# Optimization experiments

Measured on AMD Instinct MI355X. Metric: run time of the kernel, lower is better.

## Reference

```python
import jax, jax.numpy as jnp
import numpy as np

N = 100000      # num_nodes
FEAT = 256      # num_features
H = 128         # hidden
C = 40          # num_classes
K = 4           # hops
RWS = 10        # random-walk samples per node
NL = 2          # nlayer
ALPHA = 0.1


def setup_inputs() -> dict:
    key = jax.random.key(0)
    ks = jax.random.split(key, 10)
    x = jax.random.normal(ks[0], (N, FEAT), dtype=jnp.float32)
    degree = jax.random.uniform(ks[1], (N,), minval=1.0, maxval=64.0, dtype=jnp.float32)
    # precomputed random-walk endpoints per layer per hop: [NL, K, N*RWS]
    ends = jax.random.randint(ks[2], (NL, K, N * RWS), 0, N, dtype=jnp.int32)
    # att init: alpha*(1-alpha)^k, last entry (1-alpha)^K, tiled per layer
    a = ALPHA * (1.0 - ALPHA) ** jnp.arange(K + 1, dtype=jnp.float32)
    a = a.at[-1].set((1.0 - ALPHA) ** K)
    att = jnp.tile(a[None, :], (NL, 1))
    def lin(k, fan_in, fan_out):
        s = 1.0 / np.sqrt(fan_in)
        return jax.random.uniform(k, (fan_in, fan_out), minval=-s, maxval=s, dtype=jnp.float32)
    W0 = lin(ks[3], FEAT, H)
    b0 = jnp.zeros((H,), dtype=jnp.float32)
    W1 = lin(ks[4], H, H)
    b1 = jnp.zeros((H,), dtype=jnp.float32)
    W2 = lin(ks[5], H, C)
    b2 = jnp.zeros((C,), dtype=jnp.float32)
    return {"x": x, "degree": degree, "ends": ends, "att": att,
            "W0": W0, "b0": b0, "W1": W1, "b1": b1, "W2": W2, "b2": b2}


def reference(x, degree, ends, att, W0, b0, W1, b1, W2, b2):
    Ws = [(W0, b0), (W1, b1)]
    starts = jnp.repeat(jnp.arange(N), RWS)          # [N*RWS] walk start node ids
    d_sqrt = jnp.sqrt(degree)                        # degree^0.5
    d_isqrt = jax.lax.rsqrt(degree)                  # degree^-0.5
    h = x
    for i in range(NL):
        W, b = Ws[i]
        h = h @ W + b                                # Linear (dropout p=0)
        mask = att[i]                                # [K+1]
        agg = h * mask[0]
        for k in range(1, K + 1):
            e = ends[i, k - 1]                       # [N*RWS] hop-k endpoints
            w = d_sqrt[starts] * d_isqrt[e]          # degree reweighting
            samp = (w[:, None] * h[e]).reshape(N, RWS, h.shape[1]).mean(axis=1)
            agg = agg + samp * mask[k]
        h = jax.nn.relu(agg)
    logits = h @ W2 + b2
    return jax.nn.log_softmax(logits, axis=1)
```

## Files before the change

kernel.cpp:

```cpp
#include <hip/hip_runtime.h>
#include <math.h>

#define NNODES 100000
#define NFEAT  256
#define HID    128
#define NCLS   40
#define KHOP   4
#define RWSAMP 10
#define KP1    5

typedef __bf16 bf16;
typedef __attribute__((ext_vector_type(8)))  __bf16 bf16x8;
typedef __attribute__((ext_vector_type(2)))  float  f32x2;
typedef __attribute__((ext_vector_type(16))) float  f32x16;

typedef __attribute__((address_space(3))) unsigned       lds_u32;
typedef __attribute__((address_space(1))) const unsigned glb_u32;

__global__ __launch_bounds__(256) void prep_w(
    const float* __restrict__ W0, const float* __restrict__ W1,
    const float* __restrict__ W2,
    bf16* __restrict__ Wt0, bf16* __restrict__ Wt1, bf16* __restrict__ Wt2)
{
    int tid = blockIdx.x * 256 + threadIdx.x;
    if (tid < 128 * 256) {
        int n = tid >> 8, k = tid & 255;
        Wt0[tid] = (bf16)W0[k * 128 + n];
    } else if (tid < 128 * 256 + 128 * 128) {
        int i = tid - 128 * 256;
        int n = i >> 7, k = i & 127;
        Wt1[i] = (bf16)W1[k * 128 + n];
    } else if (tid < 128 * 256 + 128 * 128 + 64 * 128) {
        int i = tid - (128 * 256 + 128 * 128);
        int n = i >> 7, k = i & 127;
        Wt2[i] = (n < NCLS) ? (bf16)W2[k * NCLS + n] : (bf16)0.0f;
    }
}

template<int K, bool A_BF16>
__global__ __launch_bounds__(256) void gemm_nodes(
    const void* __restrict__ Av, const bf16* __restrict__ Wt,
    const float* __restrict__ bias, unsigned char* __restrict__ F8, int M)
{
    constexpr int BK  = 128;
    constexpr int LDB = BK + 4;
    __shared__ bf16 Bs[128 * LDB];
    __shared__ bf16 As[4][32 * LDB];

    const int tid  = threadIdx.x;
    const int wv   = tid >> 6;
    const int lane = tid & 63;
    const int l31  = lane & 31;
    const int lhi  = lane >> 5;
    const int blockRow = blockIdx.x * 128;
    const int rowBase  = blockRow + wv * 32;

    const bf16*  Ab = (const bf16*)Av;
    const float* Af = (const float*)Av;

    f32x16 acc[4];
#pragma unroll
    for (int t = 0; t < 4; ++t)
#pragma unroll
        for (int r = 0; r < 16; ++r) acc[t][r] = 0.0f;

    for (int k0 = 0; k0 < K; k0 += BK) {
        if (k0) __syncthreads();
#pragma unroll 4
        for (int l = 0; l < 8; ++l) {
            int c   = tid + l * 256;
            int row = c >> 4;
            int kc  = (c & 15) * 8;
            uint4 v = *(const uint4*)(Wt + (size_t)row * K + k0 + kc);
            *(uint2*)&Bs[row * LDB + kc]     = make_uint2(v.x, v.y);
            *(uint2*)&Bs[row * LDB + kc + 4] = make_uint2(v.z, v.w);
        }
        __syncthreads();

        if (A_BF16) {
#pragma unroll 4
            for (int l = 0; l < 8; ++l) {
                int c  = lane + l * 64;
                int r  = c >> 4;
                int kc = (c & 15) * 8;
                int gr = min(rowBase + r, M - 1);
                uint4 v = *(const uint4*)(Ab + (size_t)gr * K + k0 + kc);
                *(uint2*)&As[wv][r * LDB + kc]     = make_uint2(v.x, v.y);
                *(uint2*)&As[wv][r * LDB + kc + 4] = make_uint2(v.z, v.w);
            }
        } else {
#pragma unroll 4
            for (int l = 0; l < 16; ++l) {
                int c  = lane + l * 64;
                int r  = c >> 5;
                int kc = (c & 31) * 4;
                int gr = min(rowBase + r, M - 1);
                float4 v = *(const float4*)(Af + (size_t)gr * K + k0 + kc);
                union { bf16 h[4]; uint2 u; } t4;
                t4.h[0] = (bf16)v.x; t4.h[1] = (bf16)v.y;
                t4.h[2] = (bf16)v.z; t4.h[3] = (bf16)v.w;
                *(uint2*)&As[wv][r * LDB + kc] = t4.u;
            }
        }

#pragma unroll
        for (int ks = 0; ks < BK / 16; ++ks) {
            const int ko = ks * 16 + lhi * 8;
            union { uint2 u2[2]; bf16x8 v; } ua, ub;
            ua.u2[0] = *(const uint2*)&As[wv][l31 * LDB + ko];
            ua.u2[1] = *(const uint2*)&As[wv][l31 * LDB + ko + 4];
            bf16x8 a = ua.v;
#pragma unroll
            for (int t = 0; t < 4; ++t) {
                ub.u2[0] = *(const uint2*)&Bs[(t * 32 + l31) * LDB + ko];
                ub.u2[1] = *(const uint2*)&Bs[(t * 32 + l31) * LDB + ko + 4];
                acc[t] = __builtin_amdgcn_mfma_f32_32x32x16_bf16(a, ub.v, acc[t], 0, 0, 0);
            }
        }
    }

    __syncthreads();
    unsigned* ldsq = (unsigned*)Bs;

#pragma unroll
    for (int t = 0; t < 4; ++t) {
        int col = t * 32 + l31;
        float bc = bias[col];
#pragma unroll
        for (int G = 0; G < 4; ++G) {
            float v0 = acc[t][4 * G + 0] + bc;
            float v1 = acc[t][4 * G + 1] + bc;
            float v2 = acc[t][4 * G + 2] + bc;
            float v3 = acc[t][4 * G + 3] + bc;
            int p = __builtin_amdgcn_cvt_pk_fp8_f32(v0, v1, 0, false);
            p = __builtin_amdgcn_cvt_pk_fp8_f32(v2, v3, p, true);
            ldsq[(wv * 8 + 2 * G + lhi) * 128 + col] = (unsigned)p;
        }
    }
    __syncthreads();

    {
        const int j  = tid & 31;
        const int Q0 = (tid >> 5) * 4;
#pragma unroll
        for (int qq = 0; qq < 4; ++qq) {
            int Q = Q0 + qq;
            uint4 d = *(const uint4*)&ldsq[Q * 128 + 4 * j];
            int growb = blockRow + 4 * Q;
#pragma unroll
            for (int i = 0; i < 4; ++i) {
                unsigned sel = ((unsigned)(4 + i) << 8) | (unsigned)i;
                unsigned lo = __builtin_amdgcn_perm(d.y, d.x, sel);
                unsigned hi = __builtin_amdgcn_perm(d.w, d.z, sel);
                unsigned o  = __builtin_amdgcn_perm(hi, lo, 0x05040100u);
                if (growb + i < M)
                    *(unsigned*)(F8 + (size_t)(growb + i) * 128 + 4 * j) = o;
            }
        }
    }
}

__global__ __launch_bounds__(256) void agg_relu_fp8(
    const unsigned char* __restrict__ hf8, bf16* __restrict__ hout,
    const int* __restrict__ ends, const float* __restrict__ degree,
    const float* __restrict__ att)
{
    __shared__ __attribute__((aligned(16))) unsigned char stage[4][82 * 128];
    __shared__ int   sewE[4][82];
    __shared__ float sewW[4][82];

    const int wv   = threadIdx.x >> 6;
    const int lane = threadIdx.x & 63;
    const int n0   = blockIdx.x * 8 + wv * 2;

    for (int en = lane; en < 82; en += 64) {
        int node = en > 40;
        int j = en - node * 41;
        int n = n0 + node;
        int e;
        float w;
        if (j == 40) {
            e = n;
            w = att[0];
        } else {
            int k = j / RWSAMP, s = j - k * RWSAMP;
            e = ends[(size_t)k * (NNODES * RWSAMP) + (size_t)n * RWSAMP + s];
            w = att[k + 1] * (1.0f / RWSAMP) * sqrtf(degree[n]) * rsqrtf(degree[e]);
        }
        sewE[wv][en] = e << 7;
        sewW[wv][en] = w;
    }

    {
        const unsigned char* gbase = hf8 + (unsigned)((lane & 31) * 4);
#pragma unroll
        for (int t = 0; t < 41; ++t) {
            int r = 2 * t + (lane >> 5);
            int eoff = sewE[wv][r];
            __builtin_amdgcn_global_load_lds(
                (glb_u32*)(gbase + (unsigned)eoff),
                (lds_u32*)&stage[wv][t * 256],
                4, 0, 0);
        }
    }
    asm volatile("s_waitcnt vmcnt(0)" ::: "memory");
    __builtin_amdgcn_sched_barrier(0);

    const int q  = lane >> 4;
    const int c8 = (lane & 15) * 8;

    f32x2 a0[4], a1[4];
#pragma unroll
    for (int i = 0; i < 4; ++i) { a0[i] = (f32x2){0.f, 0.f}; a1[i] = (f32x2){0.f, 0.f}; }

#pragma unroll
    for (int t = 0; t < 10; ++t) {
        int j = 4 * t + q;
        uint2 g0 = *(const uint2*)&stage[wv][j * 128 + c8];
        uint2 g1 = *(const uint2*)&stage[wv][(41 + j) * 128 + c8];
        float w0 = sewW[wv][j];
        float w1 = sewW[wv][41 + j];
        f32x2 w20 = {w0, w0}, w21 = {w1, w1};
        a0[0] = __builtin_elementwise_fma(w20, __builtin_amdgcn_cvt_pk_f32_fp8((int)g0.x, false), a0[0]);
        a0[1] = __builtin_elementwise_fma(w20, __builtin_amdgcn_cvt_pk_f32_fp8((int)g0.x, true),  a0[1]);
        a0[2] = __builtin_elementwise_fma(w20, __builtin_amdgcn_cvt_pk_f32_fp8((int)g0.y, false), a0[2]);
        a0[3] = __builtin_elementwise_fma(w20, __builtin_amdgcn_cvt_pk_f32_fp8((int)g0.y, true),  a0[3]);
        a1[0] = __builtin_elementwise_fma(w21, __builtin_amdgcn_cvt_pk_f32_fp8((int)g1.x, false), a1[0]);
        a1[1] = __builtin_elementwise_fma(w21, __builtin_amdgcn_cvt_pk_f32_fp8((int)g1.x, true),  a1[1]);
        a1[2] = __builtin_elementwise_fma(w21, __builtin_amdgcn_cvt_pk_f32_fp8((int)g1.y, false), a1[2]);
        a1[3] = __builtin_elementwise_fma(w21, __builtin_amdgcn_cvt_pk_f32_fp8((int)g1.y, true),  a1[3]);
    }

#pragma unroll
    for (int i = 0; i < 4; ++i) {
        a0[i].x += __shfl_xor(a0[i].x, 16, 64); a0[i].y += __shfl_xor(a0[i].y, 16, 64);
        a1[i].x += __shfl_xor(a1[i].x, 16, 64); a1[i].y += __shfl_xor(a1[i].y, 16, 64);
        a0[i].x += __shfl_xor(a0[i].x, 32, 64); a0[i].y += __shfl_xor(a0[i].y, 32, 64);
        a1[i].x += __shfl_xor(a1[i].x, 32, 64); a1[i].y += __shfl_xor(a1[i].y, 32, 64);
    }

    if (q < 2) {
        const int n = n0 + q;
        f32x2* a = (q == 0) ? a0 : a1;
        const int selfRow = q ? 81 : 40;
        uint2 sv = *(const uint2*)&stage[wv][selfRow * 128 + c8];
        float att0 = sewW[wv][selfRow];
        f32x2 av = {att0, att0};
        a[0] = __builtin_elementwise_fma(av, __builtin_amdgcn_cvt_pk_f32_fp8((int)sv.x, false), a[0]);
        a[1] = __builtin_elementwise_fma(av, __builtin_amdgcn_cvt_pk_f32_fp8((int)sv.x, true),  a[1]);
        a[2] = __builtin_elementwise_fma(av, __builtin_amdgcn_cvt_pk_f32_fp8((int)sv.y, false), a[2]);
        a[3] = __builtin_elementwise_fma(av, __builtin_amdgcn_cvt_pk_f32_fp8((int)sv.y, true),  a[3]);

        f32x2 z = {0.f, 0.f};
#pragma unroll
        for (int i = 0; i < 4; ++i) a[i] = __builtin_elementwise_max(a[i], z);

        union { bf16 h[8]; uint4 u; } st;
        st.h[0] = (bf16)a[0].x; st.h[1] = (bf16)a[0].y;
        st.h[2] = (bf16)a[1].x; st.h[3] = (bf16)a[1].y;
        st.h[4] = (bf16)a[2].x; st.h[5] = (bf16)a[2].y;
        st.h[6] = (bf16)a[3].x; st.h[7] = (bf16)a[3].y;
        *(uint4*)(hout + (size_t)n * HID + c8) = st.u;
    }
}

__global__ __launch_bounds__(256) void head_mfma(
    const bf16* __restrict__ h, const bf16* __restrict__ Wt2,
    const float* __restrict__ b2, float* __restrict__ out, int M)
{
    constexpr int K = HID, LDB = K + 8;
    __shared__ bf16 Bs[64 * LDB];

    const int tid = threadIdx.x;
    constexpr int CPR = K / 8;
    for (int f = tid; f < 64 * CPR; f += 256) {
        int row = f / CPR;
        int kc  = (f % CPR) * 8;
        *(uint4*)&Bs[row * LDB + kc] = *(const uint4*)(Wt2 + (size_t)row * K + kc);
    }
    __syncthreads();

    const int wv   = tid >> 6;
    const int lane = tid & 63;
    const int l31  = lane & 31;
    const int lhi  = lane >> 5;
    const int blockRow = blockIdx.x * 128;
    const int arow = min(blockRow + wv * 32 + l31, M - 1);

    f32x16 acc[2];
#pragma unroll
    for (int t = 0; t < 2; ++t)
#pragma unroll
        for (int r = 0; r < 16; ++r) acc[t][r] = 0.0f;

#pragma unroll
    for (int ks = 0; ks < K / 16; ++ks) {
        bf16x8 a = *(const bf16x8*)(h + (size_t)arow * K + ks * 16 + lhi * 8);
#pragma unroll
        for (int t = 0; t < 2; ++t) {
            bf16x8 b = *(const bf16x8*)&Bs[(t * 32 + l31) * LDB + ks * 16 + lhi * 8];
            acc[t] = __builtin_amdgcn_mfma_f32_32x32x16_bf16(a, b, acc[t], 0, 0, 0);
        }
    }

    const float bc0 = b2[l31];
    const float bc1 = (l31 < 8) ? b2[32 + l31] : 0.0f;

#pragma unroll
    for (int r = 0; r < 16; ++r) {
        float v0 = acc[0][r] + bc0;
        float v1 = (l31 < 8) ? (acc[1][r] + bc1) : -INFINITY;

        float m = fmaxf(v0, v1);
#pragma unroll
        for (int off = 16; off > 0; off >>= 1)
            m = fmaxf(m, __shfl_xor(m, off, 64));

        float s = __expf(v0 - m) + ((l31 < 8) ? __expf(v1 - m) : 0.0f);
#pragma unroll
        for (int off = 16; off > 0; off >>= 1)
            s += __shfl_xor(s, off, 64);

        float ls = __logf(s);
        int grow = blockRow + wv * 32 + (r & 3) + 8 * (r >> 2) + 4 * lhi;
        if (grow < M) {
            out[(size_t)grow * NCLS + l31] = v0 - m - ls;
            if (l31 < 8)
                out[(size_t)grow * NCLS + 32 + l31] = v1 - m - ls;
        }
    }
}

extern "C" void kernel_launch(void* const* d_in, const int* in_sizes, int n_in,
                              void* d_out, int out_size, void* d_ws, size_t ws_size,
                              hipStream_t stream)
{
    const float* x      = (const float*)d_in[0];
    const float* degree = (const float*)d_in[1];
    const int*   ends   = (const int*)  d_in[2];
    const float* att    = (const float*)d_in[3];
    const float* W0     = (const float*)d_in[4];
    const float* b0     = (const float*)d_in[5];
    const float* W1     = (const float*)d_in[6];
    const float* b1     = (const float*)d_in[7];
    const float* W2     = (const float*)d_in[8];
    const float* b2     = (const float*)d_in[9];
    float* out = (float*)d_out;

    bf16* hb0 = (bf16*)d_ws;
    bf16* hb1 = hb0 + (size_t)NNODES * HID;
    unsigned char* hf8 = (unsigned char*)(hb1 + (size_t)NNODES * HID);
    bf16* Wt0 = (bf16*)(hf8 + (size_t)NNODES * HID);
    bf16* Wt1 = Wt0 + 128 * 256;
    bf16* Wt2 = Wt1 + 128 * 128;

    const int prepN = 128 * 256 + 128 * 128 + 64 * 128;
    prep_w<<<(prepN + 255) / 256, 256, 0, stream>>>(W0, W1, W2, Wt0, Wt1, Wt2);

    const int gGemm = (NNODES + 127) / 128;
    const int gAgg  = (NNODES + 7) / 8;

    gemm_nodes<NFEAT, false><<<gGemm, 256, 0, stream>>>(x, Wt0, b0, hf8, NNODES);
    agg_relu_fp8<<<gAgg, 256, 0, stream>>>(hf8, hb1, ends, degree, att);
    gemm_nodes<HID, true><<<gGemm, 256, 0, stream>>>(hb1, Wt1, b1, hf8, NNODES);
    agg_relu_fp8<<<gAgg, 256, 0, stream>>>(
        hf8, hb0, ends + (size_t)KHOP * NNODES * RWSAMP, degree, att + KP1);
    head_mfma<<<gGemm, 256, 0, stream>>>(hb0, Wt2, b2, out, NNODES);
}
```

Baseline: 393.9 us.

## Slice fp8 features into column slabs and gather per-slice in aggregation

The GEMM epilogue now writes the fp8 hidden features as four column slices of 32 bytes per node instead of full 128-byte rows. The aggregation kernel launches four times as many blocks, one per slice, so each pass gathers from a 3.2 MB slab that is more likely to stay cache-resident. Each slice gathers with direct 8-byte global loads and a shuffle reduction, replacing the LDS staging through global_load_lds. The cost is recomputing the endpoint indices and weights four times and issuing smaller, less coalesced gather requests.

```diff
diff --git a/kernel.cpp b/kernel.cpp
--- a/kernel.cpp
+++ b/kernel.cpp
@@ -9,13 +9,14 @@
 #define RWSAMP 10
 #define KP1    5
 
+#define NSLICE 4
+#define SLB    32
+#define NBAGG  ((NNODES + 7) / 8)
+
 typedef __bf16 bf16;
 typedef __attribute__((ext_vector_type(8)))  __bf16 bf16x8;
 typedef __attribute__((ext_vector_type(2)))  float  f32x2;
 typedef __attribute__((ext_vector_type(16))) float  f32x16;
-
-typedef __attribute__((address_space(3))) unsigned       lds_u32;
-typedef __attribute__((address_space(1))) const unsigned glb_u32;
 
 __global__ __launch_bounds__(256) void prep_w(
     const float* __restrict__ W0, const float* __restrict__ W1,
@@ -142,6 +143,8 @@
     {
         const int j  = tid & 31;
         const int Q0 = (tid >> 5) * 4;
+        const int slice = j >> 3;
+        const int b4    = (j & 7) * 4;
 #pragma unroll
         for (int qq = 0; qq < 4; ++qq) {
             int Q = Q0 + qq;
@@ -154,31 +157,32 @@
                 unsigned hi = __builtin_amdgcn_perm(d.w, d.z, sel);
                 unsigned o  = __builtin_amdgcn_perm(hi, lo, 0x05040100u);
                 if (growb + i < M)
-                    *(unsigned*)(F8 + (size_t)(growb + i) * 128 + 4 * j) = o;
+                    *(unsigned*)(F8 + ((size_t)slice * NNODES + (growb + i)) * SLB + b4) = o;
             }
         }
     }
 }
 
 __global__ __launch_bounds__(256) void agg_relu_fp8(
-    const unsigned char* __restrict__ hf8, bf16* __restrict__ hout,
+    const unsigned char* __restrict__ hf8s,
+    bf16* __restrict__ hout,
     const int* __restrict__ ends, const float* __restrict__ degree,
     const float* __restrict__ att)
 {
-    __shared__ __attribute__((aligned(16))) unsigned char stage[4][82 * 128];
-    __shared__ int   sewE[4][82];
-    __shared__ float sewW[4][82];
-
-    const int wv   = threadIdx.x >> 6;
-    const int lane = threadIdx.x & 63;
-    const int n0   = blockIdx.x * 8 + wv * 2;
+    __shared__ int   sewE[4][2][41];
+    __shared__ float sewW[4][2][41];
+
+    const int slice = blockIdx.x / NBAGG;
+    const int nb    = blockIdx.x - slice * NBAGG;
+    const int wv    = threadIdx.x >> 6;
+    const int lane  = threadIdx.x & 63;
+    const int n0    = nb * 8 + wv * 2;
 
     for (int en = lane; en < 82; en += 64) {
         int node = en > 40;
         int j = en - node * 41;
         int n = n0 + node;
-        int e;
-        float w;
+        int e; float w;
         if (j == 40) {
             e = n;
             w = att[0];
@@ -187,70 +191,44 @@
             e = ends[(size_t)k * (NNODES * RWSAMP) + (size_t)n * RWSAMP + s];
             w = att[k + 1] * (1.0f / RWSAMP) * sqrtf(degree[n]) * rsqrtf(degree[e]);
         }
-        sewE[wv][en] = e << 7;
-        sewW[wv][en] = w;
-    }
-
-    {
-        const unsigned char* gbase = hf8 + (unsigned)((lane & 31) * 4);
-#pragma unroll
-        for (int t = 0; t < 41; ++t) {
-            int r = 2 * t + (lane >> 5);
-            int eoff = sewE[wv][r];
-            __builtin_amdgcn_global_load_lds(
-                (glb_u32*)(gbase + (unsigned)eoff),
-                (lds_u32*)&stage[wv][t * 256],
-                4, 0, 0);
-        }
-    }
-    asm volatile("s_waitcnt vmcnt(0)" ::: "memory");
-    __builtin_amdgcn_sched_barrier(0);
-
-    const int q  = lane >> 4;
-    const int c8 = (lane & 15) * 8;
-
-    f32x2 a0[4], a1[4];
-#pragma unroll
-    for (int i = 0; i < 4; ++i) { a0[i] = (f32x2){0.f, 0.f}; a1[i] = (f32x2){0.f, 0.f}; }
-
-#pragma unroll
-    for (int t = 0; t < 10; ++t) {
-        int j = 4 * t + q;
-        uint2 g0 = *(const uint2*)&stage[wv][j * 128 + c8];
-        uint2 g1 = *(const uint2*)&stage[wv][(41 + j) * 128 + c8];
-        float w0 = sewW[wv][j];
-        float w1 = sewW[wv][41 + j];
-        f32x2 w20 = {w0, w0}, w21 = {w1, w1};
-        a0[0] = __builtin_elementwise_fma(w20, __builtin_amdgcn_cvt_pk_f32_fp8((int)g0.x, false), a0[0]);
-        a0[1] = __builtin_elementwise_fma(w20, __builtin_amdgcn_cvt_pk_f32_fp8((int)g0.x, true),  a0[1]);
-        a0[2] = __builtin_elementwise_fma(w20, __builtin_amdgcn_cvt_pk_f32_fp8((int)g0.y, false), a0[2]);
-        a0[3] = __builtin_elementwise_fma(w20, __builtin_amdgcn_cvt_pk_f32_fp8((int)g0.y, true),  a0[3]);
-        a1[0] = __builtin_elementwise_fma(w21, __builtin_amdgcn_cvt_pk_f32_fp8((int)g1.x, false), a1[0]);
-        a1[1] = __builtin_elementwise_fma(w21, __builtin_amdgcn_cvt_pk_f32_fp8((int)g1.x, true),  a1[1]);
-        a1[2] = __builtin_elementwise_fma(w21, __builtin_amdgcn_cvt_pk_f32_fp8((int)g1.y, false), a1[2]);
-        a1[3] = __builtin_elementwise_fma(w21, __builtin_amdgcn_cvt_pk_f32_fp8((int)g1.y, true),  a1[3]);
+        sewE[wv][node][j] = e << 5;
+        sewW[wv][node][j] = w;
+    }
+
+    const int node = lane >> 5;
+    const int g7   = (lane >> 2) & 7;
+    const int il   = lane & 3;
+    const unsigned char* sbase =
+        hf8s + (size_t)slice * ((size_t)NNODES * SLB) + il * 8;
+
+    f32x2 a[4];
+#pragma unroll
+    for (int i = 0; i < 4; ++i) a[i] = (f32x2){0.f, 0.f};
+
+#pragma unroll
+    for (int t = 0; t < 6; ++t) {
+        int j = 8 * t + g7;
+        if (j < 41) {
+            int   eo = sewE[wv][node][j];
+            float w  = sewW[wv][node][j];
+            uint2 gch = *(const uint2*)(sbase + (unsigned)eo);
+            f32x2 w2 = {w, w};
+            a[0] = __builtin_elementwise_fma(w2, __builtin_amdgcn_cvt_pk_f32_fp8((int)gch.x, false), a[0]);
+            a[1] = __builtin_elementwise_fma(w2, __builtin_amdgcn_cvt_pk_f32_fp8((int)gch.x, true),  a[1]);
+            a[2] = __builtin_elementwise_fma(w2, __builtin_amdgcn_cvt_pk_f32_fp8((int)gch.y, false), a[2]);
+            a[3] = __builtin_elementwise_fma(w2, __builtin_amdgcn_cvt_pk_f32_fp8((int)gch.y, true),  a[3]);
+        }
     }
 
 #pragma unroll
     for (int i = 0; i < 4; ++i) {
-        a0[i].x += __shfl_xor(a0[i].x, 16, 64); a0[i].y += __shfl_xor(a0[i].y, 16, 64);
-        a1[i].x += __shfl_xor(a1[i].x, 16, 64); a1[i].y += __shfl_xor(a1[i].y, 16, 64);
-        a0[i].x += __shfl_xor(a0[i].x, 32, 64); a0[i].y += __shfl_xor(a0[i].y, 32, 64);
-        a1[i].x += __shfl_xor(a1[i].x, 32, 64); a1[i].y += __shfl_xor(a1[i].y, 32, 64);
-    }
-
-    if (q < 2) {
-        const int n = n0 + q;
-        f32x2* a = (q == 0) ? a0 : a1;
-        const int selfRow = q ? 81 : 40;
-        uint2 sv = *(const uint2*)&stage[wv][selfRow * 128 + c8];
-        float att0 = sewW[wv][selfRow];
-        f32x2 av = {att0, att0};
-        a[0] = __builtin_elementwise_fma(av, __builtin_amdgcn_cvt_pk_f32_fp8((int)sv.x, false), a[0]);
-        a[1] = __builtin_elementwise_fma(av, __builtin_amdgcn_cvt_pk_f32_fp8((int)sv.x, true),  a[1]);
-        a[2] = __builtin_elementwise_fma(av, __builtin_amdgcn_cvt_pk_f32_fp8((int)sv.y, false), a[2]);
-        a[3] = __builtin_elementwise_fma(av, __builtin_amdgcn_cvt_pk_f32_fp8((int)sv.y, true),  a[3]);
-
+        a[i].x += __shfl_xor(a[i].x, 4, 64);  a[i].y += __shfl_xor(a[i].y, 4, 64);
+        a[i].x += __shfl_xor(a[i].x, 8, 64);  a[i].y += __shfl_xor(a[i].y, 8, 64);
+        a[i].x += __shfl_xor(a[i].x, 16, 64); a[i].y += __shfl_xor(a[i].y, 16, 64);
+    }
+
+    if (g7 == 0) {
+        const int n = n0 + node;
         f32x2 z = {0.f, 0.f};
 #pragma unroll
         for (int i = 0; i < 4; ++i) a[i] = __builtin_elementwise_max(a[i], z);
@@ -260,7 +238,7 @@
         st.h[2] = (bf16)a[1].x; st.h[3] = (bf16)a[1].y;
         st.h[4] = (bf16)a[2].x; st.h[5] = (bf16)a[2].y;
         st.h[6] = (bf16)a[3].x; st.h[7] = (bf16)a[3].y;
-        *(uint4*)(hout + (size_t)n * HID + c8) = st.u;
+        *(uint4*)(hout + (size_t)n * HID + slice * SLB + il * 8) = st.u;
     }
 }
 
@@ -358,7 +336,7 @@
     prep_w<<<(prepN + 255) / 256, 256, 0, stream>>>(W0, W1, W2, Wt0, Wt1, Wt2);
 
     const int gGemm = (NNODES + 127) / 128;
-    const int gAgg  = (NNODES + 7) / 8;
+    const int gAgg  = NSLICE * NBAGG;
 
     gemm_nodes<NFEAT, false><<<gGemm, 256, 0, stream>>>(x, Wt0, b0, hf8, NNODES);
     agg_relu_fp8<<<gAgg, 256, 0, stream>>>(hf8, hb1, ends, degree, att);
```

Result: slower. 526.6 us (+33.7%).
